# Optimization experiments

Hardware: AMD Instinct MI355X
Metric: run time of the kernel (lower is better)

The kernel has to match this reference:

```python
import jax, jax.numpy as jnp
import numpy as np

NUM_HEADS = 8
BLOCK_SIZE = 32   # tokens per block
WINDOW = 64       # window radius in blocks -> attends to blocks [i-64, i+64]


def setup_inputs() -> dict:
    key = jax.random.key(0)
    ks = jax.random.split(key, 5)
    B, N, C = 8, 8192, 512
    s = 0.02
    return {
        "x": jax.random.normal(ks[0], (B, N, C), dtype=jnp.float32),
        # torch Linear(dim, 3*dim): y = x @ W.T + b; we store W already transposed [in, out]
        "W_qkv": jax.random.normal(ks[1], (C, 3 * C), dtype=jnp.float32) * s,
        "b_qkv": jax.random.normal(ks[2], (3 * C,), dtype=jnp.float32) * s,
        "W_proj": jax.random.normal(ks[3], (C, C), dtype=jnp.float32) * s,
        "b_proj": jax.random.normal(ks[4], (C,), dtype=jnp.float32) * s,
    }


def reference(x, W_qkv, b_qkv, W_proj, b_proj):
    B, N, C = x.shape
    h = NUM_HEADS
    dh = C // h
    scale = jnp.asarray(dh, x.dtype) ** -0.5

    # qkv projection, then the module's head-interleaved split:
    # rearrange 'b n (h d) -> b h n d' with d = 3C/h, chunk(3) on last dim,
    # rearrange back 'b h n d -> b n (h d)'. Equivalent to:
    qkv = (x @ W_qkv + b_qkv).reshape(B, N, h, 3 * dh)
    q = qkv[..., :dh].reshape(B, N, C)
    k = qkv[..., dh:2 * dh].reshape(B, N, C)
    v = qkv[..., 2 * dh:].reshape(B, N, C)

    # dynamic blocking (N chosen divisible by BLOCK_SIZE -> no padding)
    nb = N // BLOCK_SIZE
    qb = q.reshape(B, nb, BLOCK_SIZE, C)
    kb = k.reshape(B, nb, BLOCK_SIZE, C)
    vb = v.reshape(B, nb, BLOCK_SIZE, C)

    # per-offset block attention: query block i, position s attends to
    # position s of every block j in [i-WINDOW, i+WINDOW]
    attn = jnp.einsum('bisc,bjsc->bisj', qb, kb) * scale  # [B, nb, s, nb]
    i_idx = jnp.arange(nb)[:, None]
    j_idx = jnp.arange(nb)[None, :]
    band = (j_idx >= i_idx - WINDOW) & (j_idx <= i_idx + WINDOW)  # [nb, nb]
    neg = jnp.finfo(attn.dtype).min
    attn = jnp.where(band[None, :, None, :], attn, neg)
    attn = jax.nn.softmax(attn, axis=-1)
    out = jnp.einsum('bisj,bjsc->bisc', attn, vb)  # [B, nb, s, C]
    out = out.reshape(B, N, C)

    # 'b n (h d) -> b n h d -> b n (h d)' is the identity
    return out @ W_proj + b_proj
```

## Files before the change

kernel.cpp:

```cpp
#include <hip/hip_runtime.h>
#include <hip/hip_bf16.h>
#include <stdint.h>

#define B_   8
#define N_   8192
#define C_   512
#define NB   256
#define WIN  64

typedef __attribute__((ext_vector_type(8))) short short8;
typedef __attribute__((ext_vector_type(4))) float f32x4;
typedef __hip_bfloat16 bf16;

__device__ __forceinline__ void gload_lds16(const void* g, void* l) {
  __builtin_amdgcn_global_load_lds((const __attribute__((address_space(1))) void*)g,
                                   (__attribute__((address_space(3))) void*)l, 16, 0, 0);
}

__device__ __forceinline__ f32x4 mfma16(short8 a, short8 b, f32x4 c) {
  return __builtin_amdgcn_mfma_f32_16x16x32_bf16(a, b, c, 0, 0, 0);
}


__global__ __launch_bounds__(256) void k_conv_x(const float4* __restrict__ x,
                                                ushort4* __restrict__ xb) {
  size_t idx = (size_t)blockIdx.x * 256 + threadIdx.x;
  float4 v = x[idx];
  union { ushort4 u; bf16 b[4]; } o;
  o.b[0] = __float2bfloat16(v.x); o.b[1] = __float2bfloat16(v.y);
  o.b[2] = __float2bfloat16(v.z); o.b[3] = __float2bfloat16(v.w);
  xb[idx] = o.u;
}

__global__ __launch_bounds__(256) void k_conv_w(const float* __restrict__ W,
                                                const float* __restrict__ bsrc,
                                                bf16* __restrict__ Wt,
                                                float* __restrict__ bperm,
                                                int ldw, int qkv) {
  __shared__ float tile[32][65];
  const int cc = blockIdx.x, k0 = blockIdx.y * 32;
  const int src0 = cc * 64;
  const int o0 = qkv ? ((cc % 3) * 512 + (cc / 3) * 64) : src0;
  const int tid = threadIdx.x;
#pragma unroll
  for (int q = 0; q < 8; ++q) {
    int li = q * 256 + tid;
    int r = li >> 6, c = li & 63;
    tile[r][c] = W[(size_t)(k0 + r) * ldw + src0 + c];
  }
  __syncthreads();
#pragma unroll
  for (int q = 0; q < 8; ++q) {
    int li = q * 256 + tid;
    int c2 = li >> 5, kk = li & 31;
    Wt[(size_t)(o0 + c2) * 512 + k0 + kk] = __float2bfloat16(tile[kk][c2]);
  }
  if (qkv && blockIdx.y == 0 && tid < 64) bperm[o0 + tid] = bsrc[src0 + tid];
}

#define WAITV(N) asm volatile("s_waitcnt vmcnt(" #N ")" ::: "memory")

template <int EPI>
__global__ __launch_bounds__(512, 2) void k_gemm(const bf16* __restrict__ A,
                                                 const bf16* __restrict__ Bt,
                                                 const float* __restrict__ bias,
                                                 bf16* __restrict__ qb,
                                                 bf16* __restrict__ kb,
                                                 bf16* __restrict__ vb,
                                                 float* __restrict__ outf,
                                                 int NT) {
  extern __shared__ char gsm[];
  const int tid = threadIdx.x;
  const int lane = tid & 63, wid = tid >> 6;
  const int wr = wid >> 2, wcn = wid & 3;
  const int l15 = lane & 15, l4 = lane >> 4;
  const int sx = l15 & 7;

  const int nwg = gridDim.x;
  const int cpx = nwg >> 3;
  const int swz = (blockIdx.x & 7) * cpx + (blockIdx.x >> 3);
  const int mt = swz / NT, nt = swz % NT;
  const size_t m0 = (size_t)mt * 256;
  const int n0 = nt * 256;

  f32x4 acc[8][4];
#pragma unroll
  for (int fi = 0; fi < 8; ++fi)
#pragma unroll
    for (int fj = 0; fj < 4; ++fj) acc[fi][fj] = (f32x4){0.f, 0.f, 0.f, 0.f};

#define STAGE_A(E, H, K0)                                                      \
  { _Pragma("unroll") for (int q = 0; q < 2; ++q) {                            \
      int li = q * 512 + tid;                                                  \
      int r = li >> 3, g = (li & 7) ^ (r & 7);                                 \
      gload_lds16(A + (m0 + (H) * 128 + r) * 512 + (K0) + g * 8,               \
                  gsm + (E) * 65536 + (H) * 16384 + li * 16);                  \
    } }
#define STAGE_B(E, H, K0)                                                      \
  { _Pragma("unroll") for (int q = 0; q < 2; ++q) {                            \
      int li = q * 512 + tid;                                                  \
      int r = li >> 3, g = (li & 7) ^ (r & 7);                                 \
      gload_lds16(Bt + (size_t)(n0 + (H) * 128 + r) * 512 + (K0) + g * 8,      \
                  gsm + (E) * 65536 + 32768 + (H) * 16384 + li * 16);          \
    } }

#define PHASE(FIH, FJH, LOADA, STAGE_STMT, WAIT_STMT)                          \
  {                                                                            \
    const char* Ab = gsm + d * 65536 + (FIH) * 16384;                          \
    const char* Bb = gsm + d * 65536 + 32768 + (FJH) * 16384;                  \
    if (LOADA) {                                                               \
      _Pragma("unroll") for (int f = 0; f < 4; ++f) {                          \
        int rA = f * 32 + wr * 16 + l15;                                       \
        af[f][0] = *(const short8*)(Ab + rA * 128 + ((l4 ^ sx) << 4));         \
        af[f][1] = *(const short8*)(Ab + rA * 128 + (((4 + l4) ^ sx) << 4));   \
      }                                                                        \
    }                                                                          \
    _Pragma("unroll") for (int f = 0; f < 2; ++f) {                            \
      int rB = f * 64 + wcn * 16 + l15;                                        \
      bfr[f][0] = *(const short8*)(Bb + rB * 128 + ((l4 ^ sx) << 4));          \
      bfr[f][1] = *(const short8*)(Bb + rB * 128 + (((4 + l4) ^ sx) << 4));    \
    }                                                                          \
    STAGE_STMT;                                                                \
    __builtin_amdgcn_sched_barrier(0);                                         \
    __builtin_amdgcn_s_barrier();                                              \
    __builtin_amdgcn_sched_barrier(0);                                         \
    __builtin_amdgcn_s_setprio(1);                                             \
    _Pragma("unroll") for (int f = 0; f < 4; ++f)                              \
      _Pragma("unroll") for (int g = 0; g < 2; ++g) {                          \
        acc[(FIH) * 4 + f][(FJH) * 2 + g] =                                    \
            mfma16(af[f][0], bfr[g][0], acc[(FIH) * 4 + f][(FJH) * 2 + g]);    \
        acc[(FIH) * 4 + f][(FJH) * 2 + g] =                                    \
            mfma16(af[f][1], bfr[g][1], acc[(FIH) * 4 + f][(FJH) * 2 + g]);    \
      }                                                                        \
    __builtin_amdgcn_s_setprio(0);                                             \
    __builtin_amdgcn_sched_barrier(0);                                         \
    WAIT_STMT;                                                                 \
    __builtin_amdgcn_s_barrier();                                              \
  }

  STAGE_A(0, 0, 0); STAGE_B(0, 0, 0); STAGE_B(0, 1, 0); STAGE_A(0, 1, 0);
  WAITV(4);
  __builtin_amdgcn_s_barrier();

  short8 af[4][2], bfr[2][2];
  for (int t = 0; t < 8; ++t) {
    const int d = t & 1, e = d ^ 1;
    const int kn = (t + 1) * 64;
    PHASE(0, 0, 1,
          { if (t < 7) STAGE_A(e, 0, kn); },
          { if (t < 7) { WAITV(4); } else { WAITV(2); } });
    PHASE(0, 1, 0,
          { if (t < 7) STAGE_B(e, 0, kn); },
          { if (t < 7) { WAITV(4); } else { WAITV(0); } });
    PHASE(1, 0, 1,
          { if (t < 7) STAGE_B(e, 1, kn); },
          { });
    PHASE(1, 1, 0,
          { if (t < 7) STAGE_A(e, 1, kn); },
          { if (t < 7) { WAITV(4); } });
  }
#undef PHASE
#undef STAGE_A
#undef STAGE_B

  if (EPI == 0) {
#pragma unroll
    for (int fi = 0; fi < 8; ++fi)
#pragma unroll
      for (int fj = 0; fj < 4; ++fj) {
        int o = n0 + fj * 64 + wcn * 16 + l15;
        float bia = bias[o];
        int part = o >> 9;
        int c = o & 511;
        bf16* dst = part == 0 ? qb : (part == 1 ? kb : vb);
#pragma unroll
        for (int r = 0; r < 4; ++r) {
          size_t m = m0 + fi * 32 + wr * 16 + l4 * 4 + r;
          int bidx = (int)(m >> 13);
          int n = (int)(m & 8191);
          int blk = n >> 5, s = n & 31;
          size_t di = (((size_t)(bidx * 32 + s) * 256 + blk) << 9) | c;
          dst[di] = __float2bfloat16(acc[fi][fj][r] + bia);
        }
      }
  } else {
#pragma unroll
    for (int fi = 0; fi < 8; ++fi)
#pragma unroll
      for (int fj = 0; fj < 4; ++fj) {
        int o = n0 + fj * 64 + wcn * 16 + l15;
        float bia = bias[o];
#pragma unroll
        for (int r = 0; r < 4; ++r) {
          size_t m = m0 + fi * 32 + wr * 16 + l4 * 4 + r;
          outf[m * 512 + o] = acc[fi][fj][r] + bia;
        }
      }
  }
}

__global__ __launch_bounds__(256) void k_transpose_v(const bf16* __restrict__ v,
                                                     bf16* __restrict__ vT) {
  __shared__ bf16 t[32][36];
  int bs = blockIdx.x, j0 = blockIdx.y * 32, c0 = blockIdx.z * 32;
  const bf16* src = v + (size_t)bs * NB * C_;
  bf16* dst = vT + (size_t)bs * C_ * NB;
  int r = threadIdx.x >> 3, c4 = (threadIdx.x & 7) * 4;
  *(ushort4*)&t[r][c4] = *(const ushort4*)(src + (size_t)(j0 + r) * C_ + c0 + c4);
  __syncthreads();
  union { ushort4 u; bf16 b[4]; } o;
  o.b[0] = t[c4 + 0][r]; o.b[1] = t[c4 + 1][r];
  o.b[2] = t[c4 + 2][r]; o.b[3] = t[c4 + 3][r];
  *(ushort4*)(dst + (size_t)(c0 + r) * NB + j0 + c4) = o.u;
}

#define QS_OFF   0
#define KB_OFF   32768
#define VB_OFF   98304
#define SS_OFF   131072
#define PS_OFF   135296
#define SR_OFF   137856
#define MR_OFF   141952
#define LR_OFF   142080
#define AL_OFF   142208
#define ATTN_LDS 142336

__global__ __launch_bounds__(512) void k_attn(const bf16* __restrict__ qg,
                                              const bf16* __restrict__ kg,
                                              const bf16* __restrict__ vTg,
                                              bf16* __restrict__ outb) {
  extern __shared__ char smc[];
  float* Ssf  = (float*)(smc + SS_OFF);
  bf16*  Psb  = (bf16*)(smc + PS_OFF);
  float* Sred = (float*)(smc + SR_OFF);
  float* mrow = (float*)(smc + MR_OFF);
  float* lrow = (float*)(smc + LR_OFF);
  float* alph = (float*)(smc + AL_OFF);

  const int tid = threadIdx.x, lane = tid & 63, wid = tid >> 6;
  const int l15 = lane & 15, l4 = lane >> 4;
  const int gt = (blockIdx.x & 7) * 256 + (blockIdx.x >> 3);
  const int bs = gt >> 3;
  const int b = bs >> 5, s = bs & 31;
  const int i0 = (gt & 7) * 32;
  const int jlo = max(0, i0 - WIN);
  const int jhi = min(NB - 1, i0 + 31 + WIN);
  const int nch = (jhi - jlo + 1) >> 5;
  const bf16* Qb = qg + (size_t)bs * NB * C_;
  const bf16* Kb = kg + (size_t)bs * NB * C_;
  const bf16* Vb = vTg + (size_t)bs * C_ * NB;

  const int qh_qk = (wid >> 2) & 1, jh = (wid >> 1) & 1, ks = wid & 1;
  const int qh_pv = wid >> 2, cq = wid & 3;

  f32x4 O[8];
#pragma unroll
  for (int f = 0; f < 8; ++f) O[f] = (f32x4){0.f, 0.f, 0.f, 0.f};

  if (tid < 32) { mrow[tid] = -1e30f; lrow[tid] = 0.f; }

#pragma unroll
  for (int q = 0; q < 4; ++q) {
    int li = q * 512 + tid;
    int row = li >> 6, g = (li & 63) ^ (row & 15);
    gload_lds16(Qb + (size_t)(i0 + row) * C_ + g * 8, smc + QS_OFF + li * 16);
  }
#pragma unroll
  for (int q = 0; q < 4; ++q) {
    int li = q * 512 + tid;
    int row = li >> 6, g = (li & 63) ^ (row & 15);
    gload_lds16(Kb + (size_t)(jlo + row) * C_ + g * 8, smc + KB_OFF + li * 16);
  }

  for (int t = 0; t < nch; ++t) {
    const int j0 = jlo + t * 32;
    asm volatile("s_waitcnt vmcnt(0) lgkmcnt(0)" ::: "memory");
    __builtin_amdgcn_s_barrier();
    __builtin_amdgcn_sched_barrier(0);

#pragma unroll
    for (int q = 0; q < 4; ++q) {
      int li = q * 512 + tid;
      int c = li >> 2, g = (li & 3) ^ (c & 3);
      gload_lds16(Vb + (size_t)c * NB + j0 + g * 8, smc + VB_OFF + li * 16);
    }
    if (t + 1 < nch) {
      int jn = j0 + 32;
      char* kdst = smc + KB_OFF + ((t + 1) & 1) * 32768;
#pragma unroll
      for (int q = 0; q < 4; ++q) {
        int li = q * 512 + tid;
        int row = li >> 6, g = (li & 63) ^ (row & 15);
        gload_lds16(Kb + (size_t)(jn + row) * C_ + g * 8, kdst + li * 16);
      }
    }

    {
      const int arow = qh_qk * 16 + l15;
      const int brow = jh * 16 + l15;
      const char* Qbase = smc + QS_OFF + arow * 1024;
      const char* Kbase = smc + KB_OFF + (t & 1) * 32768 + brow * 1024;
      f32x4 a0 = (f32x4){0.f, 0.f, 0.f, 0.f}, a1 = a0;
      __builtin_amdgcn_s_setprio(1);
#pragma unroll
      for (int cc = 0; cc < 8; ++cc) {
        int sa = (ks * 32 + cc * 4 + l4) ^ (arow & 15);
        int sb = (ks * 32 + cc * 4 + l4) ^ (brow & 15);
        short8 av = *(const short8*)(Qbase + sa * 16);
        short8 bv = *(const short8*)(Kbase + sb * 16);
        if (cc & 1) a1 = mfma16(av, bv, a1);
        else        a0 = mfma16(av, bv, a0);
      }
      __builtin_amdgcn_s_setprio(0);
      f32x4 acc = a0 + a1;
      if (ks) {
        *(f32x4*)&Sred[(wid >> 1) * 256 + lane * 4] = acc;
      }
      asm volatile("s_waitcnt lgkmcnt(0)" ::: "memory");
      __builtin_amdgcn_s_barrier();
      __builtin_amdgcn_sched_barrier(0);
      if (!ks) {
        f32x4 su = acc + *(f32x4*)&Sred[(wid >> 1) * 256 + lane * 4];
        int jg = j0 + jh * 16 + l15;
#pragma unroll
        for (int r = 0; r < 4; ++r) {
          int i_in = qh_qk * 16 + l4 * 4 + r;
          int i_abs = i0 + i_in;
          bool valid = (jg >= i_abs - WIN) && (jg <= i_abs + WIN);
          Ssf[i_in * 33 + jh * 16 + l15] = valid ? su[r] * 0.125f : -1e30f;
        }
      }
      asm volatile("s_waitcnt lgkmcnt(0)" ::: "memory");
      __builtin_amdgcn_s_barrier();
      __builtin_amdgcn_sched_barrier(0);
    }

    {
      int row = tid >> 4, u = tid & 15;
      float s0 = Ssf[row * 33 + u], s1 = Ssf[row * 33 + u + 16];
      float mc = fmaxf(s0, s1);
      mc = fmaxf(mc, __shfl_xor(mc, 1));
      mc = fmaxf(mc, __shfl_xor(mc, 2));
      mc = fmaxf(mc, __shfl_xor(mc, 4));
      mc = fmaxf(mc, __shfl_xor(mc, 8));
      float mo = mrow[row];
      float mn = fmaxf(mo, mc);
      float a = __expf(mo - mn);
      float p0 = __expf(s0 - mn), p1 = __expf(s1 - mn);
      float ps = p0 + p1;
      ps += __shfl_xor(ps, 1);
      ps += __shfl_xor(ps, 2);
      ps += __shfl_xor(ps, 4);
      ps += __shfl_xor(ps, 8);
      if (u == 0) {
        lrow[row] = lrow[row] * a + ps;
        mrow[row] = mn;
        alph[row] = a;
      }
      Psb[row * 40 + u] = __float2bfloat16(p0);
      Psb[row * 40 + u + 16] = __float2bfloat16(p1);
    }
    if (t + 1 < nch)
      asm volatile("s_waitcnt vmcnt(4) lgkmcnt(0)" ::: "memory");
    else
      asm volatile("s_waitcnt vmcnt(0) lgkmcnt(0)" ::: "memory");
    __builtin_amdgcn_s_barrier();
    __builtin_amdgcn_sched_barrier(0);

    {
      float ar[4];
#pragma unroll
      for (int r = 0; r < 4; ++r) ar[r] = alph[qh_pv * 16 + l4 * 4 + r];
      short8 pa = *(const short8*)(smc + PS_OFF + (qh_pv * 16 + l15) * 80 + l4 * 16);
      __builtin_amdgcn_s_setprio(1);
#pragma unroll
      for (int f = 0; f < 8; ++f) {
        int c = cq * 128 + f * 16 + l15;
        short8 vv = *(const short8*)(smc + VB_OFF + c * 64 + ((l4 ^ (c & 3)) << 4));
#pragma unroll
        for (int r = 0; r < 4; ++r) O[f][r] *= ar[r];
        O[f] = mfma16(pa, vv, O[f]);
      }
      __builtin_amdgcn_s_setprio(0);
    }
    __builtin_amdgcn_sched_barrier(0);
  }

  asm volatile("s_waitcnt lgkmcnt(0)" ::: "memory");
  __builtin_amdgcn_s_barrier();
  {
    float lr[4];
#pragma unroll
    for (int r = 0; r < 4; ++r) lr[r] = 1.f / lrow[qh_pv * 16 + l4 * 4 + r];
#pragma unroll
    for (int f = 0; f < 8; ++f) {
      int c = cq * 128 + f * 16 + l15;
#pragma unroll
      for (int r = 0; r < 4; ++r) {
        int il = qh_pv * 16 + l4 * 4 + r;
        int n = (i0 + il) * 32 + s;
        outb[((size_t)b * N_ + n) * C_ + c] = __float2bfloat16(O[f][r] * lr[r]);
      }
    }
  }
}

extern "C" void kernel_launch(void* const* d_in, const int* in_sizes, int n_in,
                              void* d_out, int out_size, void* d_ws, size_t ws_size,
                              hipStream_t stream) {
  const float* x = (const float*)d_in[0];
  const float* Wqkv = (const float*)d_in[1];
  const float* bqkv = (const float*)d_in[2];
  const float* Wproj = (const float*)d_in[3];
  const float* bproj = (const float*)d_in[4];

  char* ws = (char*)d_ws;
  const size_t SLOT = 67108864ull;
  bf16* slotA = (bf16*)ws;
  bf16* slotB = (bf16*)(ws + SLOT);
  bf16* Wqkv_t = (bf16*)(ws + 2 * SLOT);
  bf16* Wproj_t = (bf16*)(ws + 2 * SLOT + 1572864);
  float* bias_perm = (float*)(ws + 2 * SLOT + 1572864 + 524288);
  bf16* qbuf = (bf16*)d_out;
  bf16* kbuf = qbuf + 33554432ull;

  static int attr_done = 0;
  if (!attr_done) {
    hipFuncSetAttribute((const void*)k_gemm<0>,
                        hipFuncAttributeMaxDynamicSharedMemorySize, 131072);
    hipFuncSetAttribute((const void*)k_gemm<1>,
                        hipFuncAttributeMaxDynamicSharedMemorySize, 131072);
    hipFuncSetAttribute((const void*)k_attn,
                        hipFuncAttributeMaxDynamicSharedMemorySize, ATTN_LDS);
    attr_done = 1;
  }

  k_conv_x<<<32768, 256, 0, stream>>>((const float4*)x, (ushort4*)slotA);
  k_conv_w<<<dim3(24, 16), 256, 0, stream>>>(Wqkv, bqkv, Wqkv_t, bias_perm, 1536, 1);
  k_conv_w<<<dim3(8, 16), 256, 0, stream>>>(Wproj, nullptr, Wproj_t, nullptr, 512, 0);

  k_gemm<0><<<1536, 512, 131072, stream>>>(slotA, Wqkv_t, bias_perm,
                                           qbuf, kbuf, slotB, nullptr, 6);
  k_transpose_v<<<dim3(256, 8, 16), 256, 0, stream>>>(slotB, slotA);
  k_attn<<<2048, 512, ATTN_LDS, stream>>>(qbuf, kbuf, slotA, slotB);
  k_gemm<1><<<512, 512, 131072, stream>>>(slotB, Wproj_t, bproj,
                                          nullptr, nullptr, nullptr, (float*)d_out, 2);
}
```

Baseline: 328.3 us.

## Hold Q tile in registers and drop split-K reduction in QK^T stage

Q fragments are loaded once into registers by four waves instead of being staged in LDS, and each of those waves computes a full-K 16x16 score tile. This removes the cross-wave split-K partial-sum exchange and one barrier per chunk. The vmcnt wait is relaxed so the next K prefetch can stay in flight during compute. In exchange, half the waves sit idle during QK^T and those four waves carry 16 extra short8 registers, which raises register pressure; LDS use also drops.

```diff
diff --git a/kernel.cpp b/kernel.cpp
--- a/kernel.cpp
+++ b/kernel.cpp
@@ -214,16 +214,14 @@
   *(ushort4*)(dst + (size_t)(c0 + r) * NB + j0 + c4) = o.u;
 }
 
-#define QS_OFF   0
-#define KB_OFF   32768
-#define VB_OFF   98304
-#define SS_OFF   131072
-#define PS_OFF   135296
-#define SR_OFF   137856
-#define MR_OFF   141952
-#define LR_OFF   142080
-#define AL_OFF   142208
-#define ATTN_LDS 142336
+#define KB_OFF   0
+#define VB_OFF   65536
+#define SS_OFF   98304
+#define PS_OFF   102528
+#define MR_OFF   105088
+#define LR_OFF   105216
+#define AL_OFF   105344
+#define ATTN_LDS 105472
 
 __global__ __launch_bounds__(512) void k_attn(const bf16* __restrict__ qg,
                                               const bf16* __restrict__ kg,
@@ -232,7 +230,6 @@
   extern __shared__ char smc[];
   float* Ssf  = (float*)(smc + SS_OFF);
   bf16*  Psb  = (bf16*)(smc + PS_OFF);
-  float* Sred = (float*)(smc + SR_OFF);
   float* mrow = (float*)(smc + MR_OFF);
   float* lrow = (float*)(smc + LR_OFF);
   float* alph = (float*)(smc + AL_OFF);
@@ -250,7 +247,7 @@
   const bf16* Kb = kg + (size_t)bs * NB * C_;
   const bf16* Vb = vTg + (size_t)bs * C_ * NB;
 
-  const int qh_qk = (wid >> 2) & 1, jh = (wid >> 1) & 1, ks = wid & 1;
+  const int qhq = wid & 1, jhq = (wid >> 1) & 1;
   const int qh_pv = wid >> 2, cq = wid & 3;
 
   f32x4 O[8];
@@ -259,22 +256,23 @@
 
   if (tid < 32) { mrow[tid] = -1e30f; lrow[tid] = 0.f; }
 
-#pragma unroll
-  for (int q = 0; q < 4; ++q) {
-    int li = q * 512 + tid;
-    int row = li >> 6, g = (li & 63) ^ (row & 15);
-    gload_lds16(Qb + (size_t)(i0 + row) * C_ + g * 8, smc + QS_OFF + li * 16);
-  }
 #pragma unroll
   for (int q = 0; q < 4; ++q) {
     int li = q * 512 + tid;
     int row = li >> 6, g = (li & 63) ^ (row & 15);
     gload_lds16(Kb + (size_t)(jlo + row) * C_ + g * 8, smc + KB_OFF + li * 16);
   }
+  short8 qreg[16];
+  if (wid < 4) {
+    const bf16* qp = Qb + (size_t)(i0 + qhq * 16 + l15) * C_ + l4 * 8;
+#pragma unroll
+    for (int cc = 0; cc < 16; ++cc)
+      qreg[cc] = *(const short8*)(qp + cc * 32);
+  }
 
   for (int t = 0; t < nch; ++t) {
     const int j0 = jlo + t * 32;
-    asm volatile("s_waitcnt vmcnt(0) lgkmcnt(0)" ::: "memory");
+    asm volatile("s_waitcnt lgkmcnt(0)" ::: "memory");
     __builtin_amdgcn_s_barrier();
     __builtin_amdgcn_sched_barrier(0);
 
@@ -293,47 +291,39 @@
         int row = li >> 6, g = (li & 63) ^ (row & 15);
         gload_lds16(Kb + (size_t)(jn + row) * C_ + g * 8, kdst + li * 16);
       }
-    }
-
-    {
-      const int arow = qh_qk * 16 + l15;
-      const int brow = jh * 16 + l15;
-      const char* Qbase = smc + QS_OFF + arow * 1024;
+      asm volatile("s_waitcnt vmcnt(8)" ::: "memory");
+    } else {
+      asm volatile("s_waitcnt vmcnt(4)" ::: "memory");
+    }
+    __builtin_amdgcn_s_barrier();
+    __builtin_amdgcn_sched_barrier(0);
+
+    if (wid < 4) {
+      const int brow = jhq * 16 + l15;
       const char* Kbase = smc + KB_OFF + (t & 1) * 32768 + brow * 1024;
       f32x4 a0 = (f32x4){0.f, 0.f, 0.f, 0.f}, a1 = a0;
       __builtin_amdgcn_s_setprio(1);
 #pragma unroll
-      for (int cc = 0; cc < 8; ++cc) {
-        int sa = (ks * 32 + cc * 4 + l4) ^ (arow & 15);
-        int sb = (ks * 32 + cc * 4 + l4) ^ (brow & 15);
-        short8 av = *(const short8*)(Qbase + sa * 16);
+      for (int cc = 0; cc < 16; ++cc) {
+        int sb = (cc * 4 + l4) ^ (brow & 15);
         short8 bv = *(const short8*)(Kbase + sb * 16);
-        if (cc & 1) a1 = mfma16(av, bv, a1);
-        else        a0 = mfma16(av, bv, a0);
+        if (cc & 1) a1 = mfma16(qreg[cc], bv, a1);
+        else        a0 = mfma16(qreg[cc], bv, a0);
       }
       __builtin_amdgcn_s_setprio(0);
-      f32x4 acc = a0 + a1;
-      if (ks) {
-        *(f32x4*)&Sred[(wid >> 1) * 256 + lane * 4] = acc;
-      }
-      asm volatile("s_waitcnt lgkmcnt(0)" ::: "memory");
-      __builtin_amdgcn_s_barrier();
-      __builtin_amdgcn_sched_barrier(0);
-      if (!ks) {
-        f32x4 su = acc + *(f32x4*)&Sred[(wid >> 1) * 256 + lane * 4];
-        int jg = j0 + jh * 16 + l15;
-#pragma unroll
-        for (int r = 0; r < 4; ++r) {
-          int i_in = qh_qk * 16 + l4 * 4 + r;
-          int i_abs = i0 + i_in;
-          bool valid = (jg >= i_abs - WIN) && (jg <= i_abs + WIN);
-          Ssf[i_in * 33 + jh * 16 + l15] = valid ? su[r] * 0.125f : -1e30f;
-        }
-      }
-      asm volatile("s_waitcnt lgkmcnt(0)" ::: "memory");
-      __builtin_amdgcn_s_barrier();
-      __builtin_amdgcn_sched_barrier(0);
-    }
+      f32x4 su = a0 + a1;
+      int jg = j0 + jhq * 16 + l15;
+#pragma unroll
+      for (int r = 0; r < 4; ++r) {
+        int i_in = qhq * 16 + l4 * 4 + r;
+        int i_abs = i0 + i_in;
+        bool valid = (jg >= i_abs - WIN) && (jg <= i_abs + WIN);
+        Ssf[i_in * 33 + jhq * 16 + l15] = valid ? su[r] * 0.125f : -1e30f;
+      }
+    }
+    asm volatile("s_waitcnt lgkmcnt(0)" ::: "memory");
+    __builtin_amdgcn_s_barrier();
+    __builtin_amdgcn_sched_barrier(0);
 
     {
       int row = tid >> 4, u = tid & 15;
```

After: 334.6 us. About the same (+1.9%).

## Load GEMM B operand directly to registers, stage only A through LDS

Applied to the files above, without the earlier changes.

The GEMM kernel stops staging the weight (B) tile in LDS. Each wave now reads its B fragments straight from global memory into double-buffered registers, while only the A tile is double-buffered in LDS. This halves LDS use to 64 KB and replaces the four-phase schedule with one barrier per K step. The cost is more register pressure (launch bounds no longer request 2 blocks per CU), redundant global loads of B across waves, and a full vmcnt(0) wait each iteration.

```diff
diff --git a/kernel.cpp b/kernel.cpp
--- a/kernel.cpp
+++ b/kernel.cpp
@@ -61,20 +61,19 @@
 #define WAITV(N) asm volatile("s_waitcnt vmcnt(" #N ")" ::: "memory")
 
 template <int EPI>
-__global__ __launch_bounds__(512, 2) void k_gemm(const bf16* __restrict__ A,
-                                                 const bf16* __restrict__ Bt,
-                                                 const float* __restrict__ bias,
-                                                 bf16* __restrict__ qb,
-                                                 bf16* __restrict__ kb,
-                                                 bf16* __restrict__ vb,
-                                                 float* __restrict__ outf,
-                                                 int NT) {
+__global__ __launch_bounds__(512) void k_gemm(const bf16* __restrict__ A,
+                                              const bf16* __restrict__ Bt,
+                                              const float* __restrict__ bias,
+                                              bf16* __restrict__ qb,
+                                              bf16* __restrict__ kb,
+                                              bf16* __restrict__ vb,
+                                              float* __restrict__ outf,
+                                              int NT) {
   extern __shared__ char gsm[];
   const int tid = threadIdx.x;
   const int lane = tid & 63, wid = tid >> 6;
   const int wr = wid >> 2, wcn = wid & 3;
   const int l15 = lane & 15, l4 = lane >> 4;
-  const int sx = l15 & 7;
 
   const int nwg = gridDim.x;
   const int cpx = nwg >> 3;
@@ -89,79 +88,81 @@
 #pragma unroll
     for (int fj = 0; fj < 4; ++fj) acc[fi][fj] = (f32x4){0.f, 0.f, 0.f, 0.f};
 
-#define STAGE_A(E, H, K0)                                                      \
-  { _Pragma("unroll") for (int q = 0; q < 2; ++q) {                            \
+  short8 bA[4][2], bB[4][2], af[4][2];
+
+#define LOAD_B(DST, T)                                                         \
+  { _Pragma("unroll") for (int f = 0; f < 4; ++f) {                            \
+      const bf16* bp = Bt + (size_t)(n0 + f * 64 + wcn * 16 + l15) * 512 +     \
+                       (T) * 64 + l4 * 8;                                      \
+      DST[f][0] = *(const short8*)bp;                                          \
+      DST[f][1] = *(const short8*)(bp + 32);                                   \
+    } }
+
+#define STAGE_A(E, K0)                                                         \
+  { _Pragma("unroll") for (int q = 0; q < 4; ++q) {                            \
       int li = q * 512 + tid;                                                  \
       int r = li >> 3, g = (li & 7) ^ (r & 7);                                 \
-      gload_lds16(A + (m0 + (H) * 128 + r) * 512 + (K0) + g * 8,               \
-                  gsm + (E) * 65536 + (H) * 16384 + li * 16);                  \
+      gload_lds16(A + (m0 + r) * 512 + (K0) + g * 8,                           \
+                  gsm + (E) * 32768 + li * 16);                                \
     } }
-#define STAGE_B(E, H, K0)                                                      \
-  { _Pragma("unroll") for (int q = 0; q < 2; ++q) {                            \
-      int li = q * 512 + tid;                                                  \
-      int r = li >> 3, g = (li & 7) ^ (r & 7);                                 \
-      gload_lds16(Bt + (size_t)(n0 + (H) * 128 + r) * 512 + (K0) + g * 8,      \
-                  gsm + (E) * 65536 + 32768 + (H) * 16384 + li * 16);          \
-    } }
-
-#define PHASE(FIH, FJH, LOADA, STAGE_STMT, WAIT_STMT)                          \
+
+#define TILE_BODY(BCUR, BNXT, T, MORE)                                         \
   {                                                                            \
-    const char* Ab = gsm + d * 65536 + (FIH) * 16384;                          \
-    const char* Bb = gsm + d * 65536 + 32768 + (FJH) * 16384;                  \
-    if (LOADA) {                                                               \
-      _Pragma("unroll") for (int f = 0; f < 4; ++f) {                          \
-        int rA = f * 32 + wr * 16 + l15;                                       \
-        af[f][0] = *(const short8*)(Ab + rA * 128 + ((l4 ^ sx) << 4));         \
-        af[f][1] = *(const short8*)(Ab + rA * 128 + (((4 + l4) ^ sx) << 4));   \
-      }                                                                        \
+    if (MORE) {                                                                \
+      LOAD_B(BNXT, (T) + 1);                                                   \
+      STAGE_A(((T) & 1) ^ 1, ((T) + 1) * 64);                                  \
     }                                                                          \
-    _Pragma("unroll") for (int f = 0; f < 2; ++f) {                            \
-      int rB = f * 64 + wcn * 16 + l15;                                        \
-      bfr[f][0] = *(const short8*)(Bb + rB * 128 + ((l4 ^ sx) << 4));          \
-      bfr[f][1] = *(const short8*)(Bb + rB * 128 + (((4 + l4) ^ sx) << 4));    \
+    __builtin_amdgcn_sched_barrier(0);                                         \
+    const char* Ab = gsm + ((T) & 1) * 32768;                                  \
+    _Pragma("unroll") for (int f = 0; f < 4; ++f) {                            \
+      int rA = f * 32 + wr * 16 + l15;                                         \
+      af[f][0] = *(const short8*)(Ab + rA * 128 + ((l4 ^ (rA & 7)) << 4));     \
+      af[f][1] = *(const short8*)(Ab + rA * 128 + (((4 + l4) ^ (rA & 7)) << 4));\
     }                                                                          \
-    STAGE_STMT;                                                                \
-    __builtin_amdgcn_sched_barrier(0);                                         \
-    __builtin_amdgcn_s_barrier();                                              \
-    __builtin_amdgcn_sched_barrier(0);                                         \
     __builtin_amdgcn_s_setprio(1);                                             \
     _Pragma("unroll") for (int f = 0; f < 4; ++f)                              \
-      _Pragma("unroll") for (int g = 0; g < 2; ++g) {                          \
-        acc[(FIH) * 4 + f][(FJH) * 2 + g] =                                    \
-            mfma16(af[f][0], bfr[g][0], acc[(FIH) * 4 + f][(FJH) * 2 + g]);    \
-        acc[(FIH) * 4 + f][(FJH) * 2 + g] =                                    \
-            mfma16(af[f][1], bfr[g][1], acc[(FIH) * 4 + f][(FJH) * 2 + g]);    \
+      _Pragma("unroll") for (int g = 0; g < 4; ++g) {                          \
+        acc[f][g] = mfma16(af[f][0], BCUR[g][0], acc[f][g]);                   \
+        acc[f][g] = mfma16(af[f][1], BCUR[g][1], acc[f][g]);                   \
+      }                                                                        \
+    __builtin_amdgcn_s_setprio(0);                                             \
+    _Pragma("unroll") for (int f = 0; f < 4; ++f) {                            \
+      int rA = 128 + f * 32 + wr * 16 + l15;                                   \
+      af[f][0] = *(const short8*)(Ab + rA * 128 + ((l4 ^ (rA & 7)) << 4));     \
+      af[f][1] = *(const short8*)(Ab + rA * 128 + (((4 + l4) ^ (rA & 7)) << 4));\
+    }                                                                          \
+    __builtin_amdgcn_s_setprio(1);                                             \
+    _Pragma("unroll") for (int f = 0; f < 4; ++f)                              \
+      _Pragma("unroll") for (int g = 0; g < 4; ++g) {                          \
+        acc[4 + f][g] = mfma16(af[f][0], BCUR[g][0], acc[4 + f][g]);           \
+        acc[4 + f][g] = mfma16(af[f][1], BCUR[g][1], acc[4 + f][g]);           \
       }                                                                        \
     __builtin_amdgcn_s_setprio(0);                                             \
     __builtin_amdgcn_sched_barrier(0);                                         \
-    WAIT_STMT;                                                                 \
-    __builtin_amdgcn_s_barrier();                                              \
-  }
-
-  STAGE_A(0, 0, 0); STAGE_B(0, 0, 0); STAGE_B(0, 1, 0); STAGE_A(0, 1, 0);
-  WAITV(4);
+    if (MORE) {                                                                \
+      WAITV(0);                                                                \
+      asm volatile("s_waitcnt lgkmcnt(0)" ::: "memory");                       \
+      __builtin_amdgcn_s_barrier();                                            \
+      __builtin_amdgcn_sched_barrier(0);                                       \
+    }                                                                          \
+  }
+
+  LOAD_B(bA, 0);
+  STAGE_A(0, 0);
+  WAITV(0);
   __builtin_amdgcn_s_barrier();
 
-  short8 af[4][2], bfr[2][2];
-  for (int t = 0; t < 8; ++t) {
-    const int d = t & 1, e = d ^ 1;
-    const int kn = (t + 1) * 64;
-    PHASE(0, 0, 1,
-          { if (t < 7) STAGE_A(e, 0, kn); },
-          { if (t < 7) { WAITV(4); } else { WAITV(2); } });
-    PHASE(0, 1, 0,
-          { if (t < 7) STAGE_B(e, 0, kn); },
-          { if (t < 7) { WAITV(4); } else { WAITV(0); } });
-    PHASE(1, 0, 1,
-          { if (t < 7) STAGE_B(e, 1, kn); },
-          { });
-    PHASE(1, 1, 0,
-          { if (t < 7) STAGE_A(e, 1, kn); },
-          { if (t < 7) { WAITV(4); } });
-  }
-#undef PHASE
+  TILE_BODY(bA, bB, 0, true);
+  TILE_BODY(bB, bA, 1, true);
+  TILE_BODY(bA, bB, 2, true);
+  TILE_BODY(bB, bA, 3, true);
+  TILE_BODY(bA, bB, 4, true);
+  TILE_BODY(bB, bA, 5, true);
+  TILE_BODY(bA, bB, 6, true);
+  TILE_BODY(bB, bA, 7, false);
+#undef TILE_BODY
 #undef STAGE_A
-#undef STAGE_B
+#undef LOAD_B
 
   if (EPI == 0) {
 #pragma unroll
@@ -427,9 +428,9 @@
   static int attr_done = 0;
   if (!attr_done) {
     hipFuncSetAttribute((const void*)k_gemm<0>,
-                        hipFuncAttributeMaxDynamicSharedMemorySize, 131072);
+                        hipFuncAttributeMaxDynamicSharedMemorySize, 65536);
     hipFuncSetAttribute((const void*)k_gemm<1>,
-                        hipFuncAttributeMaxDynamicSharedMemorySize, 131072);
+                        hipFuncAttributeMaxDynamicSharedMemorySize, 65536);
     hipFuncSetAttribute((const void*)k_attn,
                         hipFuncAttributeMaxDynamicSharedMemorySize, ATTN_LDS);
     attr_done = 1;
@@ -439,10 +440,10 @@
   k_conv_w<<<dim3(24, 16), 256, 0, stream>>>(Wqkv, bqkv, Wqkv_t, bias_perm, 1536, 1);
   k_conv_w<<<dim3(8, 16), 256, 0, stream>>>(Wproj, nullptr, Wproj_t, nullptr, 512, 0);
 
-  k_gemm<0><<<1536, 512, 131072, stream>>>(slotA, Wqkv_t, bias_perm,
-                                           qbuf, kbuf, slotB, nullptr, 6);
+  k_gemm<0><<<1536, 512, 65536, stream>>>(slotA, Wqkv_t, bias_perm,
+                                          qbuf, kbuf, slotB, nullptr, 6);
   k_transpose_v<<<dim3(256, 8, 16), 256, 0, stream>>>(slotB, slotA);
   k_attn<<<2048, 512, ATTN_LDS, stream>>>(qbuf, kbuf, slotA, slotB);
-  k_gemm<1><<<512, 512, 131072, stream>>>(slotB, Wproj_t, bproj,
-                                          nullptr, nullptr, nullptr, (float*)d_out, 2);
-}
+  k_gemm<1><<<512, 512, 65536, stream>>>(slotB, Wproj_t, bproj,
+                                         nullptr, nullptr, nullptr, (float*)d_out, 2);
+}
```

Result: slower. 380.7 us (+15.9%).
